# Kernel optimization log

Hardware: AMD Instinct MI355X
Metric: run time of the kernel (lower is better)

Reference implementation:

```python
import jax, jax.numpy as jnp
import numpy as np

SEQ_LEN = 96
D_MODEL = 512
BATCH = 512
FREQ = SEQ_LEN // 2 + 1  # 49
EPS = 1e-5


def setup_inputs() -> dict:
    key = jax.random.key(0)
    ks = jax.random.split(key, 9)
    s = 1.0 / np.sqrt(D_MODEL)
    return {
        "x": jax.random.normal(ks[0], (BATCH, SEQ_LEN, D_MODEL), jnp.float32),
        "freq_weights": jnp.ones((FREQ,), jnp.float32),
        "Wl": jax.random.normal(ks[1], (D_MODEL, D_MODEL), jnp.float32) * s,
        "bl": jax.random.normal(ks[2], (D_MODEL,), jnp.float32) * s,
        "Wh": jax.random.normal(ks[3], (D_MODEL, D_MODEL), jnp.float32) * s,
        "bh": jax.random.normal(ks[4], (D_MODEL,), jnp.float32) * s,
        "Wg": jax.random.normal(ks[5], (2 * D_MODEL, D_MODEL), jnp.float32) * s,
        "bg": jax.random.normal(ks[6], (D_MODEL,), jnp.float32) * s,
        "gamma": jnp.ones((D_MODEL,), jnp.float32),
        "beta": jnp.zeros((D_MODEL,), jnp.float32),
    }


def reference(x, freq_weights, Wl, bl, Wh, bh, Wg, bg, gamma, beta):
    # Batched rfft over seq axis for all channels at once: [B, F, D] complex
    xf = jnp.fft.rfft(x, axis=1)
    xw = xf * freq_weights[None, :, None]
    cutoff = FREQ // 3  # 16 (static)
    idx = jnp.arange(FREQ)[None, :, None]
    x_low_f = jnp.where(idx < cutoff, xw, 0)
    x_high_f = jnp.where(idx >= cutoff, xw, 0)
    x_low = jnp.fft.irfft(x_low_f, n=SEQ_LEN, axis=1)   # [B, S, D]
    x_high = jnp.fft.irfft(x_high_f, n=SEQ_LEN, axis=1)
    x_low = jnp.einsum("bsd,de->bse", x_low, Wl) + bl
    x_high = jnp.einsum("bsd,de->bse", x_high, Wh) + bh
    gate_in = jnp.concatenate([x_low, x_high], axis=-1)  # [B, S, 2D]
    gate = jax.nn.sigmoid(jnp.einsum("bsd,de->bse", gate_in, Wg) + bg)
    out = gate * x_low + (1.0 - gate) * x_high
    y = x + out  # dropout is identity in eval mode
    mu = jnp.mean(y, axis=-1, keepdims=True)
    var = jnp.var(y, axis=-1, keepdims=True)
    return (y - mu) / jnp.sqrt(var + EPS) * gamma + beta
```

## Files before the change

### kernel.cpp

```cpp
#include <hip/hip_runtime.h>

typedef unsigned short u16;
typedef unsigned int u32;

#define SEQ 96
#define DM 512
#define NBATCH 512
#define NFREQ 49
#define CUT 16
#define MROWS (NBATCH * SEQ)

typedef __attribute__((ext_vector_type(8))) short bf16x8;
typedef __attribute__((ext_vector_type(4))) float f32x4;

__device__ __forceinline__ u16 f2bf(float f) {
  u32 u = __float_as_uint(f);
  u32 r = (u + 0x7fffu + ((u >> 16) & 1u)) >> 16;
  return (u16)r;
}
__device__ __forceinline__ float bf2f(u16 u) {
  return __uint_as_float(((u32)u) << 16);
}

__device__ __forceinline__ void g2l16(const void* g, void* l) {
  __builtin_amdgcn_global_load_lds(
      (const __attribute__((address_space(1))) void*)g,
      (__attribute__((address_space(3))) void*)l, 16, 0, 0);
}

__global__ void build_filters_k(const float* __restrict__ w,
                                u16* __restrict__ FlB, u16* __restrict__ FhB) {
  int idx = blockIdx.x * 256 + threadIdx.x;
  if (idx >= SEQ * SEQ) return;
  int s = idx / SEQ, t = idx % SEQ;
  int d = s - t;
  const float scale = 1.0f / (float)SEQ;
  const float w0 = 6.283185307179586f / (float)SEQ;
  float cl = 0.f, ch = 0.f;
  for (int k = 0; k < NFREQ; k++) {
    int m = (k * d) % SEQ;
    if (m < 0) m += SEQ;
    float c = (k == 0 || k == SEQ / 2) ? 1.0f : 2.0f;
    float v = c * w[k] * cosf(w0 * (float)m) * scale;
    if (k < CUT) cl += v; else ch += v;
  }
  FlB[idx] = f2bf(cl);
  FhB[idx] = f2bf(ch);
}

__global__ void __launch_bounds__(256) transpose_w_k(
    const float* __restrict__ W, u16* __restrict__ Wt, int K, int N) {
  __shared__ float t[32][33];
  int k0 = blockIdx.x * 32, n0 = blockIdx.y * 32;
  int tx = threadIdx.x & 31, ty = threadIdx.x >> 5;
  #pragma unroll
  for (int r = 0; r < 32; r += 8)
    t[ty + r][tx] = W[(size_t)(k0 + ty + r) * N + n0 + tx];
  __syncthreads();
  #pragma unroll
  for (int r = 0; r < 32; r += 8)
    Wt[(size_t)(n0 + ty + r) * K + k0 + tx] = f2bf(t[tx][ty + r]);
}

__global__ void __launch_bounds__(256) xt_k(
    const float* __restrict__ x, u16* __restrict__ xT) {
  __shared__ float xs[SEQ * 65];
  int b = blockIdx.x;
  int d0 = blockIdx.y * 64;
  const float* xb = x + (size_t)b * SEQ * DM + d0;
  #pragma unroll
  for (int v = 0; v < 6; v++) {
    int c = v * 256 + threadIdx.x;
    int t = c >> 4, dq = (c & 15) << 2;
    float4 f = *(const float4*)(xb + (size_t)t * DM + dq);
    xs[t * 65 + dq + 0] = f.x;
    xs[t * 65 + dq + 1] = f.y;
    xs[t * 65 + dq + 2] = f.z;
    xs[t * 65 + dq + 3] = f.w;
  }
  __syncthreads();
  u32* outw = (u32*)(xT + ((size_t)b * DM + d0) * SEQ);
  #pragma unroll
  for (int v = 0; v < 12; v++) {
    int c = v * 256 + threadIdx.x;
    int d = c / 48, tw = c % 48;
    int t0 = tw * 2;
    u32 lo = (u32)f2bf(xs[t0 * 65 + d]);
    u32 hi = (u32)f2bf(xs[(t0 + 1) * 65 + d]);
    outw[(size_t)d * 48 + tw] = lo | (hi << 16);
  }
}

__global__ void __launch_bounds__(256) filter_mfma_k(
    const u16* __restrict__ xT, const u16* __restrict__ FlB,
    const u16* __restrict__ FhB, u16* __restrict__ xl, u16* __restrict__ xh) {
  __shared__ __align__(16) u16 lds[128 * SEQ + 2 * SEQ * SEQ];
  u16* Bs = lds;
  u16* As0 = lds + 128 * SEQ;
  int tid = threadIdx.x;
  int lane = tid & 63, w = tid >> 6;
  int b = blockIdx.x, d0 = blockIdx.y * 128;

  const u16* xbase = xT + ((size_t)b * DM + d0) * SEQ;
  #pragma unroll
  for (int it = 0; it < 6; it++) {
    int c = it * 256 + tid;
    int row = c / 12, off = (c % 12) * 8;
    g2l16(xbase + (size_t)row * SEQ + off, (char*)Bs + (((it * 256 + w * 64)) << 4));
  }
  #pragma unroll
  for (int it = 0; it < 9; it++) {
    int c = it * 256 + tid;
    const u16* src = (c < 1152) ? (FlB + c * 8) : (FhB + (c - 1152) * 8);
    g2l16(src, (char*)As0 + ((it * 256 + w * 64) << 4));
  }
  __syncthreads();

  const int l15 = lane & 15, lq = lane >> 4;
  f32x4 acc[2][6][2] = {};
  #pragma unroll
  for (int ks = 0; ks < 3; ks++) {
    int kt = ks * 32;
    bf16x8 bf[2];
    #pragma unroll
    for (int j = 0; j < 2; j++)
      bf[j] = *(const bf16x8*)&Bs[(w * 32 + j * 16 + l15) * SEQ + kt + lq * 8];
    #pragma unroll
    for (int f = 0; f < 2; f++)
      #pragma unroll
      for (int i = 0; i < 6; i++) {
        bf16x8 af = *(const bf16x8*)&As0[f * SEQ * SEQ + (i * 16 + l15) * SEQ + kt + lq * 8];
        #pragma unroll
        for (int j = 0; j < 2; j++)
          acc[f][i][j] = __builtin_amdgcn_mfma_f32_16x16x32_bf16(af, bf[j], acc[f][i][j], 0, 0, 0);
      }
  }
  #pragma unroll
  for (int f = 0; f < 2; f++) {
    u16* dst = f ? xh : xl;
    #pragma unroll
    for (int i = 0; i < 6; i++)
      #pragma unroll
      for (int j = 0; j < 2; j++) {
        int d = d0 + w * 32 + j * 16 + l15;
        #pragma unroll
        for (int r = 0; r < 4; r++) {
          int s = i * 16 + lq * 4 + r;
          dst[((size_t)b * SEQ + s) * DM + d] = f2bf(acc[f][i][j][r]);
        }
      }
  }
}

__global__ void __launch_bounds__(256) gemm_proj_mfma_k(
    const u16* __restrict__ xl, const u16* __restrict__ xh,
    const u16* __restrict__ Wlt, const u16* __restrict__ Wht,
    const float* __restrict__ bl, const float* __restrict__ bh,
    u16* __restrict__ yl, u16* __restrict__ yh) {
  const u16* A = blockIdx.z ? xh : xl;
  const u16* Bt = blockIdx.z ? Wht : Wlt;
  const float* bias = blockIdx.z ? bh : bl;
  u16* C = blockIdx.z ? yh : yl;

  __shared__ __align__(16) u16 As[128 * 32];
  __shared__ __align__(16) u16 Bs[128 * 32];
  const int m0 = blockIdx.x * 128;
  const int n0 = blockIdx.y * 128;
  const int tid = threadIdx.x;
  const int lane = tid & 63;
  const int w = tid >> 6;
  const int wm = w & 1, wn = w >> 1;
  const int l15 = lane & 15;
  const int lq = lane >> 4;

  f32x4 acc[4][4] = {};

  for (int kt = 0; kt < 512; kt += 32) {
    #pragma unroll
    for (int r = 0; r < 2; r++) {
      int chunk = r * 256 + tid;
      int row = chunk >> 2;
      int ce = (chunk & 3) << 3;
      u32 lo = (u32)((r * 256 + w * 64) << 4);
      g2l16(A + (size_t)(m0 + row) * 512 + kt + ce, (char*)As + lo);
      g2l16(Bt + (size_t)(n0 + row) * 512 + kt + ce, (char*)Bs + lo);
    }
    __syncthreads();
    bf16x8 af[4], bf[4];
    #pragma unroll
    for (int i = 0; i < 4; i++)
      af[i] = *(const bf16x8*)&As[(wm * 64 + i * 16 + l15) * 32 + lq * 8];
    #pragma unroll
    for (int j = 0; j < 4; j++)
      bf[j] = *(const bf16x8*)&Bs[(wn * 64 + j * 16 + l15) * 32 + lq * 8];
    #pragma unroll
    for (int i = 0; i < 4; i++)
      #pragma unroll
      for (int j = 0; j < 4; j++)
        acc[i][j] = __builtin_amdgcn_mfma_f32_16x16x32_bf16(af[i], bf[j], acc[i][j], 0, 0, 0);
    __syncthreads();
  }

  #pragma unroll
  for (int j = 0; j < 4; j++) {
    int n = n0 + wn * 64 + j * 16 + l15;
    float bv = bias[n];
    #pragma unroll
    for (int i = 0; i < 4; i++) {
      int mrow = m0 + wm * 64 + i * 16 + lq * 4;
      #pragma unroll
      for (int r = 0; r < 4; r++)
        C[(size_t)(mrow + r) * 512 + n] = f2bf(acc[i][j][r] + bv);
    }
  }
}

__global__ void __launch_bounds__(256) gemm_gate_mfma_k(
    const u16* __restrict__ yl, const u16* __restrict__ yh,
    const u16* __restrict__ Wgt, const float* __restrict__ bg,
    u16* __restrict__ g) {
  __shared__ __align__(16) u16 As[128 * 32];
  __shared__ __align__(16) u16 Bs[128 * 32];
  const int m0 = blockIdx.x * 128;
  const int n0 = blockIdx.y * 128;
  const int tid = threadIdx.x;
  const int lane = tid & 63;
  const int w = tid >> 6;
  const int wm = w & 1, wn = w >> 1;
  const int l15 = lane & 15;
  const int lq = lane >> 4;

  f32x4 acc[4][4] = {};

  for (int kt = 0; kt < 1024; kt += 32) {
    const u16* Ak = (kt < 512) ? yl : yh;
    int ka = kt & 511;
    #pragma unroll
    for (int r = 0; r < 2; r++) {
      int chunk = r * 256 + tid;
      int row = chunk >> 2;
      int ce = (chunk & 3) << 3;
      u32 lo = (u32)((r * 256 + w * 64) << 4);
      g2l16(Ak + (size_t)(m0 + row) * 512 + ka + ce, (char*)As + lo);
      g2l16(Wgt + (size_t)(n0 + row) * 1024 + kt + ce, (char*)Bs + lo);
    }
    __syncthreads();
    bf16x8 af[4], bf[4];
    #pragma unroll
    for (int i = 0; i < 4; i++)
      af[i] = *(const bf16x8*)&As[(wm * 64 + i * 16 + l15) * 32 + lq * 8];
    #pragma unroll
    for (int j = 0; j < 4; j++)
      bf[j] = *(const bf16x8*)&Bs[(wn * 64 + j * 16 + l15) * 32 + lq * 8];
    #pragma unroll
    for (int i = 0; i < 4; i++)
      #pragma unroll
      for (int j = 0; j < 4; j++)
        acc[i][j] = __builtin_amdgcn_mfma_f32_16x16x32_bf16(af[i], bf[j], acc[i][j], 0, 0, 0);
    __syncthreads();
  }

  #pragma unroll
  for (int j = 0; j < 4; j++) {
    int n = n0 + wn * 64 + j * 16 + l15;
    float bv = bg[n];
    #pragma unroll
    for (int i = 0; i < 4; i++) {
      int mrow = m0 + wm * 64 + i * 16 + lq * 4;
      #pragma unroll
      for (int r = 0; r < 4; r++) {
        float z = acc[i][j][r] + bv;
        g[(size_t)(mrow + r) * 512 + n] = f2bf(1.0f / (1.0f + __expf(-z)));
      }
    }
  }
}

__global__ void __launch_bounds__(256) final_ln_k(
    const float* __restrict__ x, const u16* __restrict__ yl,
    const u16* __restrict__ yh, const u16* __restrict__ g,
    const float* __restrict__ gamma, const float* __restrict__ beta,
    float* __restrict__ out) {
  __shared__ float red[8];
  int r = blockIdx.x;
  size_t base = (size_t)r * 512;
  float vv[2];
  float sum = 0.f, sumsq = 0.f;
  #pragma unroll
  for (int j = 0; j < 2; j++) {
    int e = threadIdx.x + j * 256;
    float lv = bf2f(yl[base + e]);
    float hv = bf2f(yh[base + e]);
    float gv = bf2f(g[base + e]);
    float v = x[base + e] + gv * lv + (1.f - gv) * hv;
    vv[j] = v;
    sum += v;
    sumsq += v * v;
  }
  #pragma unroll
  for (int off = 32; off; off >>= 1) {
    sum += __shfl_down(sum, off);
    sumsq += __shfl_down(sumsq, off);
  }
  int wid = threadIdx.x >> 6;
  if ((threadIdx.x & 63) == 0) {
    red[wid] = sum;
    red[4 + wid] = sumsq;
  }
  __syncthreads();
  sum = red[0] + red[1] + red[2] + red[3];
  sumsq = red[4] + red[5] + red[6] + red[7];
  float mu = sum * (1.f / 512.f);
  float var = sumsq * (1.f / 512.f) - mu * mu;
  float inv = rsqrtf(var + 1e-5f);
  #pragma unroll
  for (int j = 0; j < 2; j++) {
    int e = threadIdx.x + j * 256;
    out[base + e] = (vv[j] - mu) * inv * gamma[e] + beta[e];
  }
}

extern "C" void kernel_launch(void* const* d_in, const int* in_sizes, int n_in,
                              void* d_out, int out_size, void* d_ws, size_t ws_size,
                              hipStream_t stream) {
  const float* x     = (const float*)d_in[0];
  const float* fw    = (const float*)d_in[1];
  const float* Wl    = (const float*)d_in[2];
  const float* bl    = (const float*)d_in[3];
  const float* Wh    = (const float*)d_in[4];
  const float* bh    = (const float*)d_in[5];
  const float* Wg    = (const float*)d_in[6];
  const float* bg    = (const float*)d_in[7];
  const float* gamma = (const float*)d_in[8];
  const float* beta  = (const float*)d_in[9];
  float* out = (float*)d_out;

  char* ws = (char*)d_ws;
  u16* FlB = (u16*)ws;
  u16* FhB = FlB + SEQ * SEQ;
  u16* Wlt = (u16*)(ws + 64 * 1024);
  u16* Wht = Wlt + 512 * 512;
  u16* Wgt = Wht + 512 * 512;
  size_t tsz = (size_t)MROWS * 512;
  u16* xl = (u16*)(ws + 4 * 1024 * 1024);
  u16* xh = xl + tsz;
  u16* yl = xh + tsz;
  u16* yh = yl + tsz;
  u16* xT = yl;
  u16* gbuf = xl;

  build_filters_k<<<dim3(36), dim3(256), 0, stream>>>(fw, FlB, FhB);
  transpose_w_k<<<dim3(16, 16), dim3(256), 0, stream>>>(Wl, Wlt, 512, 512);
  transpose_w_k<<<dim3(16, 16), dim3(256), 0, stream>>>(Wh, Wht, 512, 512);
  transpose_w_k<<<dim3(32, 16), dim3(256), 0, stream>>>(Wg, Wgt, 1024, 512);
  xt_k<<<dim3(NBATCH, DM / 64), dim3(256), 0, stream>>>(x, xT);
  filter_mfma_k<<<dim3(NBATCH, DM / 128), dim3(256), 0, stream>>>(xT, FlB, FhB, xl, xh);
  gemm_proj_mfma_k<<<dim3(MROWS / 128, 4, 2), dim3(256), 0, stream>>>(
      xl, xh, Wlt, Wht, bl, bh, yl, yh);
  gemm_gate_mfma_k<<<dim3(MROWS / 128, 4), dim3(256), 0, stream>>>(yl, yh, Wgt, bg, gbuf);
  final_ln_k<<<dim3(MROWS), dim3(256), 0, stream>>>(x, yl, yh, gbuf, gamma, beta, out);
}
```

Baseline: 458.4 us.

## Reorder projection before spectral filter and widen GEMM K-tile

Uses linearity to swap the order of operations: x is first cast to bf16 and projected by the concatenated [Wl|Wh] in one GEMM. The result is written transposed (seq-major per channel), and then the low- and high-pass filter matrices are applied along the sequence axis with bias added afterwards. This removes the separate transpose kernel and merges the two projection GEMMs into one launch that reads the A operand once. The K-tile of both GEMMs also goes from 32 to 64, halving the number of barriers. In exchange, the transposed 2-byte stores scattered in the projection epilogue may be poorly coalesced, and LDS use rises.

```diff
diff --git a/kernel.cpp b/kernel.cpp
--- a/kernel.cpp
+++ b/kernel.cpp
@@ -62,108 +62,24 @@
     Wt[(size_t)(n0 + ty + r) * K + k0 + tx] = f2bf(t[tx][ty + r]);
 }
 
-__global__ void __launch_bounds__(256) xt_k(
-    const float* __restrict__ x, u16* __restrict__ xT) {
-  __shared__ float xs[SEQ * 65];
-  int b = blockIdx.x;
-  int d0 = blockIdx.y * 64;
-  const float* xb = x + (size_t)b * SEQ * DM + d0;
-  #pragma unroll
-  for (int v = 0; v < 6; v++) {
-    int c = v * 256 + threadIdx.x;
-    int t = c >> 4, dq = (c & 15) << 2;
-    float4 f = *(const float4*)(xb + (size_t)t * DM + dq);
-    xs[t * 65 + dq + 0] = f.x;
-    xs[t * 65 + dq + 1] = f.y;
-    xs[t * 65 + dq + 2] = f.z;
-    xs[t * 65 + dq + 3] = f.w;
-  }
-  __syncthreads();
-  u32* outw = (u32*)(xT + ((size_t)b * DM + d0) * SEQ);
-  #pragma unroll
-  for (int v = 0; v < 12; v++) {
-    int c = v * 256 + threadIdx.x;
-    int d = c / 48, tw = c % 48;
-    int t0 = tw * 2;
-    u32 lo = (u32)f2bf(xs[t0 * 65 + d]);
-    u32 hi = (u32)f2bf(xs[(t0 + 1) * 65 + d]);
-    outw[(size_t)d * 48 + tw] = lo | (hi << 16);
-  }
-}
-
-__global__ void __launch_bounds__(256) filter_mfma_k(
-    const u16* __restrict__ xT, const u16* __restrict__ FlB,
-    const u16* __restrict__ FhB, u16* __restrict__ xl, u16* __restrict__ xh) {
-  __shared__ __align__(16) u16 lds[128 * SEQ + 2 * SEQ * SEQ];
-  u16* Bs = lds;
-  u16* As0 = lds + 128 * SEQ;
-  int tid = threadIdx.x;
-  int lane = tid & 63, w = tid >> 6;
-  int b = blockIdx.x, d0 = blockIdx.y * 128;
-
-  const u16* xbase = xT + ((size_t)b * DM + d0) * SEQ;
-  #pragma unroll
-  for (int it = 0; it < 6; it++) {
-    int c = it * 256 + tid;
-    int row = c / 12, off = (c % 12) * 8;
-    g2l16(xbase + (size_t)row * SEQ + off, (char*)Bs + (((it * 256 + w * 64)) << 4));
-  }
-  #pragma unroll
-  for (int it = 0; it < 9; it++) {
-    int c = it * 256 + tid;
-    const u16* src = (c < 1152) ? (FlB + c * 8) : (FhB + (c - 1152) * 8);
-    g2l16(src, (char*)As0 + ((it * 256 + w * 64) << 4));
-  }
-  __syncthreads();
-
-  const int l15 = lane & 15, lq = lane >> 4;
-  f32x4 acc[2][6][2] = {};
-  #pragma unroll
-  for (int ks = 0; ks < 3; ks++) {
-    int kt = ks * 32;
-    bf16x8 bf[2];
-    #pragma unroll
-    for (int j = 0; j < 2; j++)
-      bf[j] = *(const bf16x8*)&Bs[(w * 32 + j * 16 + l15) * SEQ + kt + lq * 8];
-    #pragma unroll
-    for (int f = 0; f < 2; f++)
-      #pragma unroll
-      for (int i = 0; i < 6; i++) {
-        bf16x8 af = *(const bf16x8*)&As0[f * SEQ * SEQ + (i * 16 + l15) * SEQ + kt + lq * 8];
-        #pragma unroll
-        for (int j = 0; j < 2; j++)
-          acc[f][i][j] = __builtin_amdgcn_mfma_f32_16x16x32_bf16(af, bf[j], acc[f][i][j], 0, 0, 0);
-      }
-  }
-  #pragma unroll
-  for (int f = 0; f < 2; f++) {
-    u16* dst = f ? xh : xl;
-    #pragma unroll
-    for (int i = 0; i < 6; i++)
-      #pragma unroll
-      for (int j = 0; j < 2; j++) {
-        int d = d0 + w * 32 + j * 16 + l15;
-        #pragma unroll
-        for (int r = 0; r < 4; r++) {
-          int s = i * 16 + lq * 4 + r;
-          dst[((size_t)b * SEQ + s) * DM + d] = f2bf(acc[f][i][j][r]);
-        }
-      }
-  }
-}
-
-__global__ void __launch_bounds__(256) gemm_proj_mfma_k(
-    const u16* __restrict__ xl, const u16* __restrict__ xh,
-    const u16* __restrict__ Wlt, const u16* __restrict__ Wht,
-    const float* __restrict__ bl, const float* __restrict__ bh,
-    u16* __restrict__ yl, u16* __restrict__ yh) {
-  const u16* A = blockIdx.z ? xh : xl;
-  const u16* Bt = blockIdx.z ? Wht : Wlt;
-  const float* bias = blockIdx.z ? bh : bl;
-  u16* C = blockIdx.z ? yh : yl;
-
-  __shared__ __align__(16) u16 As[128 * 32];
-  __shared__ __align__(16) u16 Bs[128 * 32];
+__global__ void __launch_bounds__(256) xb_k(const float* __restrict__ x,
+                                            u16* __restrict__ xb) {
+  size_t t = ((size_t)blockIdx.x * 256 + threadIdx.x) * 8;
+  float4 f0 = *(const float4*)(x + t);
+  float4 f1 = *(const float4*)(x + t + 4);
+  uint4 o;
+  o.x = (u32)f2bf(f0.x) | ((u32)f2bf(f0.y) << 16);
+  o.y = (u32)f2bf(f0.z) | ((u32)f2bf(f0.w) << 16);
+  o.z = (u32)f2bf(f1.x) | ((u32)f2bf(f1.y) << 16);
+  o.w = (u32)f2bf(f1.z) | ((u32)f2bf(f1.w) << 16);
+  *(uint4*)(xb + t) = o;
+}
+
+__global__ void __launch_bounds__(256) proj_dual_k(
+    const u16* __restrict__ xb, const u16* __restrict__ Wt,
+    u16* __restrict__ uT, u16* __restrict__ vT) {
+  __shared__ __align__(16) u16 As[128 * 64];
+  __shared__ __align__(16) u16 Bs[128 * 64];
   const int m0 = blockIdx.x * 128;
   const int n0 = blockIdx.y * 128;
   const int tid = threadIdx.x;
@@ -175,43 +91,118 @@
 
   f32x4 acc[4][4] = {};
 
-  for (int kt = 0; kt < 512; kt += 32) {
-    #pragma unroll
-    for (int r = 0; r < 2; r++) {
-      int chunk = r * 256 + tid;
-      int row = chunk >> 2;
-      int ce = (chunk & 3) << 3;
+  for (int kt = 0; kt < 512; kt += 64) {
+    #pragma unroll
+    for (int r = 0; r < 4; r++) {
+      int c = r * 256 + tid;
+      int row = c >> 3;
+      int off = (c & 7) << 3;
       u32 lo = (u32)((r * 256 + w * 64) << 4);
-      g2l16(A + (size_t)(m0 + row) * 512 + kt + ce, (char*)As + lo);
-      g2l16(Bt + (size_t)(n0 + row) * 512 + kt + ce, (char*)Bs + lo);
+      g2l16(xb + (size_t)(m0 + row) * 512 + kt + off, (char*)As + lo);
+      g2l16(Wt + (size_t)(n0 + row) * 512 + kt + off, (char*)Bs + lo);
     }
     __syncthreads();
-    bf16x8 af[4], bf[4];
-    #pragma unroll
-    for (int i = 0; i < 4; i++)
-      af[i] = *(const bf16x8*)&As[(wm * 64 + i * 16 + l15) * 32 + lq * 8];
-    #pragma unroll
-    for (int j = 0; j < 4; j++)
-      bf[j] = *(const bf16x8*)&Bs[(wn * 64 + j * 16 + l15) * 32 + lq * 8];
-    #pragma unroll
-    for (int i = 0; i < 4; i++)
+    #pragma unroll
+    for (int kk = 0; kk < 64; kk += 32) {
+      bf16x8 af[4], bf[4];
+      #pragma unroll
+      for (int i = 0; i < 4; i++)
+        af[i] = *(const bf16x8*)&As[(wm * 64 + i * 16 + l15) * 64 + kk + lq * 8];
       #pragma unroll
       for (int j = 0; j < 4; j++)
-        acc[i][j] = __builtin_amdgcn_mfma_f32_16x16x32_bf16(af[i], bf[j], acc[i][j], 0, 0, 0);
+        bf[j] = *(const bf16x8*)&Bs[(wn * 64 + j * 16 + l15) * 64 + kk + lq * 8];
+      #pragma unroll
+      for (int i = 0; i < 4; i++)
+        #pragma unroll
+        for (int j = 0; j < 4; j++)
+          acc[i][j] = __builtin_amdgcn_mfma_f32_16x16x32_bf16(af[i], bf[j], acc[i][j], 0, 0, 0);
+    }
     __syncthreads();
   }
 
   #pragma unroll
   for (int j = 0; j < 4; j++) {
-    int n = n0 + wn * 64 + j * 16 + l15;
-    float bv = bias[n];
+    int nv = n0 + wn * 64 + j * 16 + l15;
+    u16* dst = (nv < 512) ? uT : vT;
+    int e = nv & 511;
     #pragma unroll
     for (int i = 0; i < 4; i++) {
-      int mrow = m0 + wm * 64 + i * 16 + lq * 4;
-      #pragma unroll
-      for (int r = 0; r < 4; r++)
-        C[(size_t)(mrow + r) * 512 + n] = f2bf(acc[i][j][r] + bv);
-    }
+      int mbase = m0 + wm * 64 + i * 16 + lq * 4;
+      int b = mbase / 96, s = mbase % 96;
+      ushort4 st;
+      st.x = f2bf(acc[i][j][0]);
+      st.y = f2bf(acc[i][j][1]);
+      st.z = f2bf(acc[i][j][2]);
+      st.w = f2bf(acc[i][j][3]);
+      *(ushort4*)&dst[((size_t)b * 512 + e) * SEQ + s] = st;
+    }
+  }
+}
+
+__global__ void __launch_bounds__(256) filter2_k(
+    const u16* __restrict__ uT, const u16* __restrict__ vT,
+    const u16* __restrict__ FlB, const u16* __restrict__ FhB,
+    const float* __restrict__ bl, const float* __restrict__ bh,
+    u16* __restrict__ yl, u16* __restrict__ yh) {
+  __shared__ __align__(16) u16 lds[2 * SEQ * SEQ + 2 * 64 * SEQ];
+  u16* Fls = lds;
+  u16* Bu = lds + 2 * SEQ * SEQ;
+  u16* Bv = Bu + 64 * SEQ;
+  const int tid = threadIdx.x;
+  const int lane = tid & 63, w = tid >> 6;
+  const int b = blockIdx.x, d0 = blockIdx.y * 64;
+
+  #pragma unroll
+  for (int it = 0; it < 9; it++) {
+    int c = it * 256 + tid;
+    const u16* src = (c < 1152) ? (FlB + c * 8) : (FhB + (c - 1152) * 8);
+    g2l16(src, (char*)Fls + ((it * 256 + w * 64) << 4));
+  }
+  const u16* bu = uT + ((size_t)b * 512 + d0) * SEQ;
+  const u16* bv = vT + ((size_t)b * 512 + d0) * SEQ;
+  #pragma unroll
+  for (int it = 0; it < 3; it++) {
+    int c = it * 256 + tid;
+    int row = c / 12, off = (c % 12) * 8;
+    u32 lo = (u32)((it * 256 + w * 64) << 4);
+    g2l16(bu + (size_t)row * SEQ + off, (char*)Bu + lo);
+    g2l16(bv + (size_t)row * SEQ + off, (char*)Bv + lo);
+  }
+  __syncthreads();
+
+  const int wf = w >> 1, wd = w & 1;
+  const int l15 = lane & 15, lq = lane >> 4;
+  const u16* F = wf ? (Fls + SEQ * SEQ) : Fls;
+  const u16* Bsrc = wf ? Bv : Bu;
+  f32x4 acc[6][2] = {};
+  #pragma unroll
+  for (int ks = 0; ks < 3; ks++) {
+    int kt = ks * 32;
+    bf16x8 bf[2];
+    #pragma unroll
+    for (int j = 0; j < 2; j++)
+      bf[j] = *(const bf16x8*)&Bsrc[(wd * 32 + j * 16 + l15) * SEQ + kt + lq * 8];
+    #pragma unroll
+    for (int i = 0; i < 6; i++) {
+      bf16x8 af = *(const bf16x8*)&F[(i * 16 + l15) * SEQ + kt + lq * 8];
+      #pragma unroll
+      for (int j = 0; j < 2; j++)
+        acc[i][j] = __builtin_amdgcn_mfma_f32_16x16x32_bf16(af, bf[j], acc[i][j], 0, 0, 0);
+    }
+  }
+  const float* bias = wf ? bh : bl;
+  u16* dst = wf ? yh : yl;
+  #pragma unroll
+  for (int j = 0; j < 2; j++) {
+    int d = d0 + wd * 32 + j * 16 + l15;
+    float bv2 = bias[d];
+    #pragma unroll
+    for (int i = 0; i < 6; i++)
+      #pragma unroll
+      for (int r = 0; r < 4; r++) {
+        int s = i * 16 + lq * 4 + r;
+        dst[((size_t)b * SEQ + s) * DM + d] = f2bf(acc[i][j][r] + bv2);
+      }
   }
 }
 
@@ -219,8 +210,8 @@
     const u16* __restrict__ yl, const u16* __restrict__ yh,
     const u16* __restrict__ Wgt, const float* __restrict__ bg,
     u16* __restrict__ g) {
-  __shared__ __align__(16) u16 As[128 * 32];
-  __shared__ __align__(16) u16 Bs[128 * 32];
+  __shared__ __align__(16) u16 As[128 * 64];
+  __shared__ __align__(16) u16 Bs[128 * 64];
   const int m0 = blockIdx.x * 128;
   const int n0 = blockIdx.y * 128;
   const int tid = threadIdx.x;
@@ -232,31 +223,34 @@
 
   f32x4 acc[4][4] = {};
 
-  for (int kt = 0; kt < 1024; kt += 32) {
+  for (int kt = 0; kt < 1024; kt += 64) {
     const u16* Ak = (kt < 512) ? yl : yh;
     int ka = kt & 511;
     #pragma unroll
-    for (int r = 0; r < 2; r++) {
-      int chunk = r * 256 + tid;
-      int row = chunk >> 2;
-      int ce = (chunk & 3) << 3;
+    for (int r = 0; r < 4; r++) {
+      int c = r * 256 + tid;
+      int row = c >> 3;
+      int off = (c & 7) << 3;
       u32 lo = (u32)((r * 256 + w * 64) << 4);
-      g2l16(Ak + (size_t)(m0 + row) * 512 + ka + ce, (char*)As + lo);
-      g2l16(Wgt + (size_t)(n0 + row) * 1024 + kt + ce, (char*)Bs + lo);
+      g2l16(Ak + (size_t)(m0 + row) * 512 + ka + off, (char*)As + lo);
+      g2l16(Wgt + (size_t)(n0 + row) * 1024 + kt + off, (char*)Bs + lo);
     }
     __syncthreads();
-    bf16x8 af[4], bf[4];
-    #pragma unroll
-    for (int i = 0; i < 4; i++)
-      af[i] = *(const bf16x8*)&As[(wm * 64 + i * 16 + l15) * 32 + lq * 8];
-    #pragma unroll
-    for (int j = 0; j < 4; j++)
-      bf[j] = *(const bf16x8*)&Bs[(wn * 64 + j * 16 + l15) * 32 + lq * 8];
-    #pragma unroll
-    for (int i = 0; i < 4; i++)
+    #pragma unroll
+    for (int kk = 0; kk < 64; kk += 32) {
+      bf16x8 af[4], bf[4];
+      #pragma unroll
+      for (int i = 0; i < 4; i++)
+        af[i] = *(const bf16x8*)&As[(wm * 64 + i * 16 + l15) * 64 + kk + lq * 8];
       #pragma unroll
       for (int j = 0; j < 4; j++)
-        acc[i][j] = __builtin_amdgcn_mfma_f32_16x16x32_bf16(af[i], bf[j], acc[i][j], 0, 0, 0);
+        bf[j] = *(const bf16x8*)&Bs[(wn * 64 + j * 16 + l15) * 64 + kk + lq * 8];
+      #pragma unroll
+      for (int i = 0; i < 4; i++)
+        #pragma unroll
+        for (int j = 0; j < 4; j++)
+          acc[i][j] = __builtin_amdgcn_mfma_f32_16x16x32_bf16(af[i], bf[j], acc[i][j], 0, 0, 0);
+    }
     __syncthreads();
   }
 
@@ -338,25 +332,24 @@
   char* ws = (char*)d_ws;
   u16* FlB = (u16*)ws;
   u16* FhB = FlB + SEQ * SEQ;
-  u16* Wlt = (u16*)(ws + 64 * 1024);
-  u16* Wht = Wlt + 512 * 512;
-  u16* Wgt = Wht + 512 * 512;
+  u16* Wt  = (u16*)(ws + 64 * 1024);
+  u16* Wgt = Wt + 1024 * 512;
   size_t tsz = (size_t)MROWS * 512;
-  u16* xl = (u16*)(ws + 4 * 1024 * 1024);
-  u16* xh = xl + tsz;
-  u16* yl = xh + tsz;
-  u16* yh = yl + tsz;
-  u16* xT = yl;
-  u16* gbuf = xl;
+  u16* xb = (u16*)(ws + 4 * 1024 * 1024);
+  u16* uT = xb + tsz;
+  u16* vT = uT + tsz;
+  u16* yh = vT + tsz;
+  u16* yl = xb;
+  u16* gb = uT;
 
   build_filters_k<<<dim3(36), dim3(256), 0, stream>>>(fw, FlB, FhB);
-  transpose_w_k<<<dim3(16, 16), dim3(256), 0, stream>>>(Wl, Wlt, 512, 512);
-  transpose_w_k<<<dim3(16, 16), dim3(256), 0, stream>>>(Wh, Wht, 512, 512);
+  transpose_w_k<<<dim3(16, 16), dim3(256), 0, stream>>>(Wl, Wt, 512, 512);
+  transpose_w_k<<<dim3(16, 16), dim3(256), 0, stream>>>(Wh, Wt + 512 * 512, 512, 512);
   transpose_w_k<<<dim3(32, 16), dim3(256), 0, stream>>>(Wg, Wgt, 1024, 512);
-  xt_k<<<dim3(NBATCH, DM / 64), dim3(256), 0, stream>>>(x, xT);
-  filter_mfma_k<<<dim3(NBATCH, DM / 128), dim3(256), 0, stream>>>(xT, FlB, FhB, xl, xh);
-  gemm_proj_mfma_k<<<dim3(MROWS / 128, 4, 2), dim3(256), 0, stream>>>(
-      xl, xh, Wlt, Wht, bl, bh, yl, yh);
-  gemm_gate_mfma_k<<<dim3(MROWS / 128, 4), dim3(256), 0, stream>>>(yl, yh, Wgt, bg, gbuf);
-  final_ln_k<<<dim3(MROWS), dim3(256), 0, stream>>>(x, yl, yh, gbuf, gamma, beta, out);
-}
+  xb_k<<<dim3(MROWS * 512 / 2048), dim3(256), 0, stream>>>(x, xb);
+  proj_dual_k<<<dim3(MROWS / 128, 8), dim3(256), 0, stream>>>(xb, Wt, uT, vT);
+  filter2_k<<<dim3(NBATCH, DM / 64), dim3(256), 0, stream>>>(
+      uT, vT, FlB, FhB, bl, bh, yl, yh);
+  gemm_gate_mfma_k<<<dim3(MROWS / 128, 4), dim3(256), 0, stream>>>(yl, yh, Wgt, bg, gb);
+  final_ln_k<<<dim3(MROWS), dim3(256), 0, stream>>>(x, yl, yh, gb, gamma, beta, out);
+}
```

New measurement: 494.3 us. 7.8% more time.
